# Optimization experiments

Hardware: AMD Instinct MI355X
Metric: run time of the kernel (lower is better)

## Reference

```python
import jax, jax.numpy as jnp
import numpy as np

SPARSE_DEGREE = 4   # MUL_LEV_SPA_ATN_SPARSE_DEGREES[level=1]
NUM_HEADS = 16


def setup_inputs() -> dict:
    key = jax.random.key(0)
    k1, k2, k3 = jax.random.split(key, 3)
    S, B, H, Dh = 4096, 2, NUM_HEADS, 128  # [seq, batch, heads, head_dim]
    q = jax.random.normal(k1, (S, B, H, Dh), jnp.float32)
    k = jax.random.normal(k2, (S, B, H, Dh), jnp.float32)
    v = jax.random.normal(k3, (S, B, H, Dh), jnp.float32)
    return {"q": q, "k": k, "v": v}


def reference(q, k, v):
    # Single-device (world_size=1) MLSAForOneLevel forward, is_prompt=True.
    d = SPARSE_DEGREE
    S, B, H, Dh = q.shape
    Ssp = S // d  # number of sparse tokens per head

    # Per-head strided indices: head h selects tokens h%d, h%d+d, ...  -> [Ssp, H]
    idx = (jnp.arange(H) % d)[None, :] + d * jnp.arange(Ssp)[:, None]
    idx4 = jnp.broadcast_to(idx[:, None, :, None], (Ssp, B, H, Dh))
    gather0 = lambda x: jnp.take_along_axis(x, idx4, axis=0)
    q_ = gather0(q)  # prompt phase: q is also sparsified
    k_ = gather0(k)
    v_ = gather0(v)

    # Core attention (causal), layout [t, b, h, d]
    scale = 1.0 / jnp.sqrt(jnp.asarray(Dh, q.dtype))
    scores = jnp.einsum('tbhd,sbhd->bhts', q_, k_) * scale  # [B,H,Ssp,Ssp]
    causal = jnp.tril(jnp.ones((Ssp, Ssp), bool))
    scores = jnp.where(causal[None, None], scores, -jnp.inf)
    m = jnp.max(scores, axis=-1, keepdims=True)
    e = jnp.exp(scores - m)
    denom = jnp.sum(e, axis=-1, keepdims=True)          # softmax denominator [B,H,Ssp,1]
    probs = e / denom
    ctx = jnp.einsum('bhts,sbhd->tbhd', probs, v_)       # [Ssp,B,H,Dh]

    # Reconstruction scatter: rc_indices[token, h] = i where token = i*d + h%d, else Ssp (-> zero row)
    rc = jnp.full((S, H), Ssp, jnp.int32)
    rc = rc.at[idx, jnp.arange(H)[None, :]].set(jnp.arange(Ssp, dtype=jnp.int32)[:, None])
    padded = jnp.concatenate([ctx, jnp.zeros((1, B, H, Dh), ctx.dtype)], axis=0)
    rc4 = jnp.broadcast_to(rc[:, None, :, None], (S, B, H, Dh))
    out = jnp.take_along_axis(padded, rc4, axis=0)       # [S,B,H,Dh]

    denomi = jnp.transpose(denom, (2, 0, 1, 3)).astype(jnp.float32)  # 'b h t x -> t b h x'
    return out, denomi
```

## Files before the change

kernel.cpp:

```cpp
#include <hip/hip_runtime.h>
#include <hip/hip_bf16.h>

typedef __attribute__((ext_vector_type(8))) __bf16 bf16x8;
typedef __attribute__((ext_vector_type(4))) float f32x4;

#define S_TOK 4096
#define NB 2
#define NH 16
#define DH 128
#define DEG 4
#define SSP 1024
#define QB 64
#define KB 64
#define NQT (SSP / QB)
#define TOKS (NB * NH * DH)
#define SCALE 0.08838834764831845f
#define VP 132

union U8 {
  bf16x8 v;
  unsigned u[4];
  unsigned short s[8];
};

__device__ __forceinline__ unsigned short f2bfu(float x) {
  __bf16 b = (__bf16)x;
  return __builtin_bit_cast(unsigned short, b);
}
__device__ __forceinline__ unsigned pkbf(float lo, float hi) {
  return (unsigned)f2bfu(lo) | ((unsigned)f2bfu(hi) << 16);
}

__global__ __launch_bounds__(256, 2) void mlsa_fused(
    const float* __restrict__ Qg, const float* __restrict__ Kg,
    const float* __restrict__ Vg, float* __restrict__ Og,
    float* __restrict__ Dg) {
  __shared__ __align__(16) char lds[KB * 256 + DH * VP];
  char* KL = lds;
  char* VT = lds + KB * 256;

  const int bid = blockIdx.x;
  const int jperm = bid >> 5;
  const int qt = (jperm < 8) ? jperm : 23 - jperm;
  const int bh = bid & 31;
  const int b = bh >> 4;
  const int h = bh & 15;
  const int hm4 = h & 3;
  const int tid = (int)threadIdx.x;
  const int wv = tid >> 6;
  const int ln = tid & 63;
  const int g = ln >> 4;
  const int c = ln & 15;
  const size_t bhoff = (size_t)b * (NH * DH) + (size_t)h * DH;

  const int qbase = qt * QB + wv * 16;
  const int q_sp = qbase + c;

  const int krow = tid >> 2;
  const int kd0 = (tid & 3) * 8;
  const int vd4 = tid & 31;
  const int vsp = tid >> 5;

  f32x4 qraw[8];
  {
    const float* qrow = Qg + (size_t)(q_sp * DEG + hm4) * TOKS + bhoff + g * 8;
    #pragma unroll
    for (int dc = 0; dc < 4; ++dc) {
      qraw[2 * dc] = *(const f32x4*)(qrow + dc * 32);
      qraw[2 * dc + 1] = *(const f32x4*)(qrow + dc * 32 + 4);
    }
  }
  f32x4 kreg[8], vreg[8];
  {
    const float* kr = Kg + (size_t)(krow * DEG + hm4) * TOKS + bhoff + kd0;
    #pragma unroll
    for (int p4 = 0; p4 < 4; ++p4) {
      kreg[2 * p4] = *(const f32x4*)(kr + p4 * 32);
      kreg[2 * p4 + 1] = *(const f32x4*)(kr + p4 * 32 + 4);
    }
    #pragma unroll
    for (int pp = 0; pp < 4; ++pp) {
      int s = pp * 16 + vsp * 2;
      const float* vr = Vg + (size_t)(s * DEG + hm4) * TOKS + bhoff + vd4 * 4;
      vreg[2 * pp] = *(const f32x4*)vr;
      vreg[2 * pp + 1] = *(const f32x4*)(vr + (size_t)DEG * TOKS);
    }
  }

  {
    const f32x4 z = {0.f, 0.f, 0.f, 0.f};
    for (int u = 0; u < 24; ++u) {
      int fid = u * 256 + tid;
      int row = fid >> 5;
      int col = fid & 31;
      int rr = row >> 6;
      int qi = qt * QB + (row & 63);
      int off = (hm4 + 1 + rr) & 3;
      *(f32x4*)(Og + (size_t)(qi * DEG + off) * TOKS + bhoff + col * 4) = z;
    }
  }

  bf16x8 qf[4];
  #pragma unroll
  for (int dc = 0; dc < 4; ++dc) {
    U8 t;
    #pragma unroll
    for (int i = 0; i < 4; ++i) {
      t.s[i] = f2bfu(qraw[2 * dc][i] * SCALE);
      t.s[4 + i] = f2bfu(qraw[2 * dc + 1][i] * SCALE);
    }
    qf[dc] = t.v;
  }

  U8 kpk[4];
  unsigned vpk[4][4];
  auto conv = [&]() {
    #pragma unroll
    for (int p4 = 0; p4 < 4; ++p4) {
      #pragma unroll
      for (int i = 0; i < 4; ++i) {
        kpk[p4].s[i] = f2bfu(kreg[2 * p4][i]);
        kpk[p4].s[4 + i] = f2bfu(kreg[2 * p4 + 1][i]);
      }
    }
    #pragma unroll
    for (int pp = 0; pp < 4; ++pp) {
      #pragma unroll
      for (int j = 0; j < 4; ++j)
        vpk[pp][j] = pkbf(vreg[2 * pp][j], vreg[2 * pp + 1][j]);
    }
  };
  auto wr = [&]() {
    #pragma unroll
    for (int p4 = 0; p4 < 4; ++p4) {
      int d = kd0 + p4 * 32;
      int byte = (krow * 256 + d * 2) ^ ((krow & 7) << 4);
      *(bf16x8*)(KL + byte) = kpk[p4].v;
    }
    #pragma unroll
    for (int pp = 0; pp < 4; ++pp) {
      int s = pp * 16 + vsp * 2;
      #pragma unroll
      for (int j = 0; j < 4; ++j)
        *(unsigned*)(VT + (vd4 * 4 + j) * VP + s * 2) = vpk[pp][j];
    }
  };

  conv();
  wr();
  __syncthreads();

  float m_run = -1e30f, m_true = -1e30f, l_run = 0.f;
  f32x4 acc[8];
  #pragma unroll
  for (int i = 0; i < 8; ++i) acc[i] = (f32x4){0.f, 0.f, 0.f, 0.f};

  for (int kt = 0; kt <= qt; ++kt) {
    const bool pf = (kt < qt);
    if (pf) {
      const float* kr =
          Kg + (size_t)(((kt + 1) * KB + krow) * DEG + hm4) * TOKS + bhoff + kd0;
      #pragma unroll
      for (int p4 = 0; p4 < 4; ++p4) {
        kreg[2 * p4] = *(const f32x4*)(kr + p4 * 32);
        kreg[2 * p4 + 1] = *(const f32x4*)(kr + p4 * 32 + 4);
      }
      #pragma unroll
      for (int pp = 0; pp < 4; ++pp) {
        int s = (kt + 1) * KB + pp * 16 + vsp * 2;
        const float* vr = Vg + (size_t)(s * DEG + hm4) * TOKS + bhoff + vd4 * 4;
        vreg[2 * pp] = *(const f32x4*)vr;
        vreg[2 * pp + 1] = *(const f32x4*)(vr + (size_t)DEG * TOKS);
      }
      __builtin_amdgcn_sched_barrier(0);
    }

    const int cbmax = pf ? 3 : wv;
    f32x4 sc[4];
    #pragma unroll
    for (int cb = 0; cb < 4; ++cb) sc[cb] = (f32x4){0.f, 0.f, 0.f, 0.f};
    #pragma unroll
    for (int cb = 0; cb < 4; ++cb) {
      if (cb <= cbmax) {
        int rbase = (cb * 16 + c) * 256;
        int sw = (c & 7) << 4;
        #pragma unroll
        for (int dc = 0; dc < 4; ++dc) {
          int byte = (rbase + (dc * 32 + g * 8) * 2) ^ sw;
          bf16x8 kf = *(const bf16x8*)(KL + byte);
          sc[cb] = __builtin_amdgcn_mfma_f32_16x16x32_bf16(kf, qf[dc], sc[cb], 0, 0, 0);
        }
      }
    }

    float p[4][4];
    float mt = -1e30f;
    if (pf) {
      #pragma unroll
      for (int cb = 0; cb < 4; ++cb) {
        #pragma unroll
        for (int r = 0; r < 4; ++r) {
          float v = sc[cb][r];
          p[cb][r] = v;
          mt = fmaxf(mt, v);
        }
      }
    } else {
      const int qloc = wv * 16 + c;
      #pragma unroll
      for (int cb = 0; cb < 4; ++cb) {
        #pragma unroll
        for (int r = 0; r < 4; ++r) {
          int kloc = cb * 16 + g * 4 + r;
          float v = (cb <= cbmax && kloc <= qloc) ? sc[cb][r] : -1e30f;
          p[cb][r] = v;
          mt = fmaxf(mt, v);
        }
      }
    }
    mt = fmaxf(mt, __shfl_xor(mt, 16));
    mt = fmaxf(mt, __shfl_xor(mt, 32));
    m_true = fmaxf(m_true, mt);

    float resc = 1.0f;
    if (!__all(mt <= m_run + 8.0f)) {
      float m_new = fmaxf(m_run, mt);
      resc = __expf(m_run - m_new);
      m_run = m_new;
      #pragma unroll
      for (int r = 0; r < 4; ++r) {
        float f = __shfl(resc, g * 4 + r);
        #pragma unroll
        for (int db = 0; db < 8; ++db) acc[db][r] *= f;
      }
    }
    float ls = 0.f;
    #pragma unroll
    for (int cb = 0; cb < 4; ++cb) {
      #pragma unroll
      for (int r = 0; r < 4; ++r) {
        float e = __expf(p[cb][r] - m_run);
        p[cb][r] = e;
        ls += e;
      }
    }
    ls += __shfl_xor(ls, 16);
    ls += __shfl_xor(ls, 32);
    l_run = l_run * resc + ls;

    unsigned pk2[4][2];
    #pragma unroll
    for (int cb = 0; cb < 4; ++cb) {
      pk2[cb][0] = pkbf(p[cb][0], p[cb][1]);
      pk2[cb][1] = pkbf(p[cb][2], p[cb][3]);
    }
    const int srcA = c + 16 * ((2 * g) & 3);
    const int srcB = c + 16 * ((2 * g + 1) & 3);
    const bool hi = (g & 2) != 0;
    const int sbmax = pf ? 1 : (wv >> 1);
    #pragma unroll
    for (int sb = 0; sb < 2; ++sb) {
      if (sb <= sbmax) {
        unsigned a0 = (unsigned)__shfl((int)pk2[2 * sb][0], srcA);
        unsigned b0 = (unsigned)__shfl((int)pk2[2 * sb + 1][0], srcA);
        unsigned a1 = (unsigned)__shfl((int)pk2[2 * sb][1], srcA);
        unsigned b1 = (unsigned)__shfl((int)pk2[2 * sb + 1][1], srcA);
        unsigned a2 = (unsigned)__shfl((int)pk2[2 * sb][0], srcB);
        unsigned b2 = (unsigned)__shfl((int)pk2[2 * sb + 1][0], srcB);
        unsigned a3 = (unsigned)__shfl((int)pk2[2 * sb][1], srcB);
        unsigned b3 = (unsigned)__shfl((int)pk2[2 * sb + 1][1], srcB);
        U8 pa;
        pa.u[0] = hi ? b0 : a0;
        pa.u[1] = hi ? b1 : a1;
        pa.u[2] = hi ? b2 : a2;
        pa.u[3] = hi ? b3 : a3;
        #pragma unroll
        for (int db = 0; db < 8; ++db) {
          int byte = (db * 16 + c) * VP + (sb * 32 + g * 8) * 2;
          U8 vb;
          vb.u[0] = *(const unsigned*)(VT + byte);
          vb.u[1] = *(const unsigned*)(VT + byte + 4);
          vb.u[2] = *(const unsigned*)(VT + byte + 8);
          vb.u[3] = *(const unsigned*)(VT + byte + 12);
          acc[db] = __builtin_amdgcn_mfma_f32_16x16x32_bf16(pa.v, vb.v, acc[db], 0, 0, 0);
        }
      }
    }

    if (!pf) break;
    conv();
    __syncthreads();
    wr();
    __syncthreads();
  }

  float inv = 1.0f / l_run;
  #pragma unroll
  for (int r = 0; r < 4; ++r) {
    float fi = __shfl(inv, g * 4 + r);
    int q2 = qbase + g * 4 + r;
    float* orow = Og + (size_t)(q2 * DEG + hm4) * TOKS + bhoff;
    #pragma unroll
    for (int db = 0; db < 8; ++db) orow[db * 16 + c] = acc[db][r] * fi;
  }
  if (g == 0)
    Dg[(size_t)(qbase + c) * (NB * NH) + b * NH + h] =
        l_run * __expf(m_run - m_true);
}

extern "C" void kernel_launch(void* const* d_in, const int* in_sizes, int n_in,
                              void* d_out, int out_size, void* d_ws, size_t ws_size,
                              hipStream_t stream) {
  (void)in_sizes; (void)n_in; (void)out_size; (void)d_ws; (void)ws_size;
  const float* q = (const float*)d_in[0];
  const float* k = (const float*)d_in[1];
  const float* v = (const float*)d_in[2];
  float* out = (float*)d_out;
  float* den = out + (size_t)S_TOK * NB * NH * DH;
  mlsa_fused<<<dim3(NQT * NB * NH), dim3(256), 0, stream>>>(q, k, v, out, den);
}
```

Measured before the change: 208.4 us.

## Split head dim across blocks, pair causal q-tiles, double-buffer K/V in LDS

Each block now handles one 64-wide half of the value head dimension and processes two causal query tiles (j and 15-j) back to back, which balances work per block. K/V staging moves to a double-buffered LDS layout, so each iteration needs one barrier instead of two, and the first K/V tile for the second phase is prefetched. The trade-off is that QK^T scores are computed twice, once per dh-half. That doubles QK MFMA work and K loads in exchange for better balance and overlap.

```diff
diff --git a/kernel.cpp b/kernel.cpp
--- a/kernel.cpp
+++ b/kernel.cpp
@@ -12,10 +12,12 @@
 #define SSP 1024
 #define QB 64
 #define KB 64
-#define NQT (SSP / QB)
 #define TOKS (NB * NH * DH)
 #define SCALE 0.08838834764831845f
-#define VP 132
+#define VP 148
+#define KSZ (KB * 256)
+#define VSZ (64 * VP)
+#define BUFSZ (KSZ + VSZ)
 
 union U8 {
   bf16x8 v;
@@ -35,14 +37,12 @@
     const float* __restrict__ Qg, const float* __restrict__ Kg,
     const float* __restrict__ Vg, float* __restrict__ Og,
     float* __restrict__ Dg) {
-  __shared__ __align__(16) char lds[KB * 256 + DH * VP];
-  char* KL = lds;
-  char* VT = lds + KB * 256;
+  __shared__ __align__(16) char lds[2 * BUFSZ];
 
   const int bid = blockIdx.x;
-  const int jperm = bid >> 5;
-  const int qt = (jperm < 8) ? jperm : 23 - jperm;
   const int bh = bid & 31;
+  const int j = (bid >> 5) & 7;
+  const int dhv = bid >> 8;
   const int b = bh >> 4;
   const int h = bh & 15;
   const int hm4 = h & 3;
@@ -52,68 +52,34 @@
   const int g = ln >> 4;
   const int c = ln & 15;
   const size_t bhoff = (size_t)b * (NH * DH) + (size_t)h * DH;
-
-  const int qbase = qt * QB + wv * 16;
-  const int q_sp = qbase + c;
+  const int dbase = dhv * 64;
 
   const int krow = tid >> 2;
   const int kd0 = (tid & 3) * 8;
-  const int vd4 = tid & 31;
-  const int vsp = tid >> 5;
-
-  f32x4 qraw[8];
-  {
-    const float* qrow = Qg + (size_t)(q_sp * DEG + hm4) * TOKS + bhoff + g * 8;
-    #pragma unroll
-    for (int dc = 0; dc < 4; ++dc) {
-      qraw[2 * dc] = *(const f32x4*)(qrow + dc * 32);
-      qraw[2 * dc + 1] = *(const f32x4*)(qrow + dc * 32 + 4);
-    }
-  }
-  f32x4 kreg[8], vreg[8];
-  {
-    const float* kr = Kg + (size_t)(krow * DEG + hm4) * TOKS + bhoff + kd0;
+  const int vd4 = tid & 15;
+  const int vsp = tid >> 4;
+
+  f32x4 kreg[8], vreg[4];
+  auto issue_kv = [&](int kt) {
+    const float* kr =
+        Kg + (size_t)((kt * KB + krow) * DEG + hm4) * TOKS + bhoff + kd0;
     #pragma unroll
     for (int p4 = 0; p4 < 4; ++p4) {
       kreg[2 * p4] = *(const f32x4*)(kr + p4 * 32);
       kreg[2 * p4 + 1] = *(const f32x4*)(kr + p4 * 32 + 4);
     }
     #pragma unroll
-    for (int pp = 0; pp < 4; ++pp) {
-      int s = pp * 16 + vsp * 2;
-      const float* vr = Vg + (size_t)(s * DEG + hm4) * TOKS + bhoff + vd4 * 4;
+    for (int pp = 0; pp < 2; ++pp) {
+      int s = kt * KB + pp * 32 + vsp * 2;
+      const float* vr =
+          Vg + (size_t)(s * DEG + hm4) * TOKS + bhoff + dbase + vd4 * 4;
       vreg[2 * pp] = *(const f32x4*)vr;
       vreg[2 * pp + 1] = *(const f32x4*)(vr + (size_t)DEG * TOKS);
     }
-  }
-
-  {
-    const f32x4 z = {0.f, 0.f, 0.f, 0.f};
-    for (int u = 0; u < 24; ++u) {
-      int fid = u * 256 + tid;
-      int row = fid >> 5;
-      int col = fid & 31;
-      int rr = row >> 6;
-      int qi = qt * QB + (row & 63);
-      int off = (hm4 + 1 + rr) & 3;
-      *(f32x4*)(Og + (size_t)(qi * DEG + off) * TOKS + bhoff + col * 4) = z;
-    }
-  }
-
-  bf16x8 qf[4];
-  #pragma unroll
-  for (int dc = 0; dc < 4; ++dc) {
-    U8 t;
-    #pragma unroll
-    for (int i = 0; i < 4; ++i) {
-      t.s[i] = f2bfu(qraw[2 * dc][i] * SCALE);
-      t.s[4 + i] = f2bfu(qraw[2 * dc + 1][i] * SCALE);
-    }
-    qf[dc] = t.v;
-  }
+  };
 
   U8 kpk[4];
-  unsigned vpk[4][4];
+  unsigned vpk[2][4];
   auto conv = [&]() {
     #pragma unroll
     for (int p4 = 0; p4 < 4; ++p4) {
@@ -124,13 +90,15 @@
       }
     }
     #pragma unroll
-    for (int pp = 0; pp < 4; ++pp) {
-      #pragma unroll
-      for (int j = 0; j < 4; ++j)
-        vpk[pp][j] = pkbf(vreg[2 * pp][j], vreg[2 * pp + 1][j]);
+    for (int pp = 0; pp < 2; ++pp) {
+      #pragma unroll
+      for (int jj = 0; jj < 4; ++jj)
+        vpk[pp][jj] = pkbf(vreg[2 * pp][jj], vreg[2 * pp + 1][jj]);
     }
   };
-  auto wr = [&]() {
+  auto wr = [&](int buf) {
+    char* KL = lds + buf * BUFSZ;
+    char* VT = KL + KSZ;
     #pragma unroll
     for (int p4 = 0; p4 < 4; ++p4) {
       int d = kd0 + p4 * 32;
@@ -138,174 +106,221 @@
       *(bf16x8*)(KL + byte) = kpk[p4].v;
     }
     #pragma unroll
-    for (int pp = 0; pp < 4; ++pp) {
-      int s = pp * 16 + vsp * 2;
-      #pragma unroll
-      for (int j = 0; j < 4; ++j)
-        *(unsigned*)(VT + (vd4 * 4 + j) * VP + s * 2) = vpk[pp][j];
+    for (int pp = 0; pp < 2; ++pp) {
+      int s2 = (pp * 32 + vsp * 2) * 2;
+      #pragma unroll
+      for (int jj = 0; jj < 4; ++jj)
+        *(unsigned*)(VT + (vd4 * 4 + jj) * VP + s2) = vpk[pp][jj];
     }
   };
 
-  conv();
-  wr();
-  __syncthreads();
-
-  float m_run = -1e30f, m_true = -1e30f, l_run = 0.f;
-  f32x4 acc[8];
-  #pragma unroll
-  for (int i = 0; i < 8; ++i) acc[i] = (f32x4){0.f, 0.f, 0.f, 0.f};
-
-  for (int kt = 0; kt <= qt; ++kt) {
-    const bool pf = (kt < qt);
-    if (pf) {
-      const float* kr =
-          Kg + (size_t)(((kt + 1) * KB + krow) * DEG + hm4) * TOKS + bhoff + kd0;
-      #pragma unroll
-      for (int p4 = 0; p4 < 4; ++p4) {
-        kreg[2 * p4] = *(const f32x4*)(kr + p4 * 32);
-        kreg[2 * p4 + 1] = *(const f32x4*)(kr + p4 * 32 + 4);
-      }
-      #pragma unroll
-      for (int pp = 0; pp < 4; ++pp) {
-        int s = (kt + 1) * KB + pp * 16 + vsp * 2;
-        const float* vr = Vg + (size_t)(s * DEG + hm4) * TOKS + bhoff + vd4 * 4;
-        vreg[2 * pp] = *(const f32x4*)vr;
-        vreg[2 * pp + 1] = *(const f32x4*)(vr + (size_t)DEG * TOKS);
-      }
-      __builtin_amdgcn_sched_barrier(0);
-    }
-
-    const int cbmax = pf ? 3 : wv;
-    f32x4 sc[4];
-    #pragma unroll
-    for (int cb = 0; cb < 4; ++cb) sc[cb] = (f32x4){0.f, 0.f, 0.f, 0.f};
-    #pragma unroll
-    for (int cb = 0; cb < 4; ++cb) {
-      if (cb <= cbmax) {
-        int rbase = (cb * 16 + c) * 256;
-        int sw = (c & 7) << 4;
+  int cur = 0;
+
+  for (int ph = 0; ph < 2; ++ph) {
+    const int qt = ph ? (15 - j) : j;
+    const int qbase = qt * QB + wv * 16;
+    const int q_sp = qbase + c;
+
+    f32x4 qraw[8];
+    {
+      const float* qrow =
+          Qg + (size_t)(q_sp * DEG + hm4) * TOKS + bhoff + g * 8;
+      #pragma unroll
+      for (int dc = 0; dc < 4; ++dc) {
+        qraw[2 * dc] = *(const f32x4*)(qrow + dc * 32);
+        qraw[2 * dc + 1] = *(const f32x4*)(qrow + dc * 32 + 4);
+      }
+    }
+
+    if (ph == 0) {
+      issue_kv(0);
+      const f32x4 z = {0.f, 0.f, 0.f, 0.f};
+      for (int u = 0; u < 24; ++u) {
+        int fid = u * 256 + tid;
+        int col = fid & 15;
+        int row = fid >> 4;
+        int t2 = row >= 192;
+        int r2 = row - (t2 ? 192 : 0);
+        int rr = r2 >> 6;
+        int qi = (t2 ? (15 - j) : j) * QB + (r2 & 63);
+        int off = (hm4 + 1 + rr) & 3;
+        *(f32x4*)(Og + (size_t)(qi * DEG + off) * TOKS + bhoff + dbase +
+                  col * 4) = z;
+      }
+    }
+
+    bf16x8 qf[4];
+    #pragma unroll
+    for (int dc = 0; dc < 4; ++dc) {
+      U8 t;
+      #pragma unroll
+      for (int i = 0; i < 4; ++i) {
+        t.s[i] = f2bfu(qraw[2 * dc][i] * SCALE);
+        t.s[4 + i] = f2bfu(qraw[2 * dc + 1][i] * SCALE);
+      }
+      qf[dc] = t.v;
+    }
+
+    if (ph == 0) {
+      conv();
+      wr(0);
+      __syncthreads();
+      cur = 0;
+    }
+
+    float m_run = -1e30f, m_true = -1e30f, l_run = 0.f;
+    f32x4 acc[4];
+    #pragma unroll
+    for (int i = 0; i < 4; ++i) acc[i] = (f32x4){0.f, 0.f, 0.f, 0.f};
+
+    for (int kt = 0; kt <= qt; ++kt) {
+      const bool diag = (kt == qt);
+      const bool has_next = (kt < qt) || (ph == 0);
+      if (has_next) {
+        issue_kv(diag ? 0 : kt + 1);
+        __builtin_amdgcn_sched_barrier(0);
+      }
+
+      const char* KL = lds + cur * BUFSZ;
+      const char* VT = KL + KSZ;
+
+      const int cbmax = diag ? wv : 3;
+      f32x4 sc[4];
+      #pragma unroll
+      for (int cb = 0; cb < 4; ++cb) sc[cb] = (f32x4){0.f, 0.f, 0.f, 0.f};
+      #pragma unroll
+      for (int cb = 0; cb < 4; ++cb) {
+        if (cb <= cbmax) {
+          int rbase = (cb * 16 + c) * 256;
+          int sw = (c & 7) << 4;
+          #pragma unroll
+          for (int dc = 0; dc < 4; ++dc) {
+            int byte = (rbase + (dc * 32 + g * 8) * 2) ^ sw;
+            bf16x8 kf = *(const bf16x8*)(KL + byte);
+            sc[cb] =
+                __builtin_amdgcn_mfma_f32_16x16x32_bf16(kf, qf[dc], sc[cb], 0, 0, 0);
+          }
+        }
+      }
+
+      float p[4][4];
+      float mt = -1e30f;
+      if (!diag) {
         #pragma unroll
-        for (int dc = 0; dc < 4; ++dc) {
-          int byte = (rbase + (dc * 32 + g * 8) * 2) ^ sw;
-          bf16x8 kf = *(const bf16x8*)(KL + byte);
-          sc[cb] = __builtin_amdgcn_mfma_f32_16x16x32_bf16(kf, qf[dc], sc[cb], 0, 0, 0);
-        }
-      }
-    }
-
-    float p[4][4];
-    float mt = -1e30f;
-    if (pf) {
+        for (int cb = 0; cb < 4; ++cb) {
+          #pragma unroll
+          for (int r = 0; r < 4; ++r) {
+            float v = sc[cb][r];
+            p[cb][r] = v;
+            mt = fmaxf(mt, v);
+          }
+        }
+      } else {
+        const int qloc = wv * 16 + c;
+        #pragma unroll
+        for (int cb = 0; cb < 4; ++cb) {
+          #pragma unroll
+          for (int r = 0; r < 4; ++r) {
+            int kloc = cb * 16 + g * 4 + r;
+            float v = (cb <= cbmax && kloc <= qloc) ? sc[cb][r] : -1e30f;
+            p[cb][r] = v;
+            mt = fmaxf(mt, v);
+          }
+        }
+      }
+      mt = fmaxf(mt, __shfl_xor(mt, 16));
+      mt = fmaxf(mt, __shfl_xor(mt, 32));
+      m_true = fmaxf(m_true, mt);
+
+      float resc = 1.0f;
+      if (!__all(mt <= m_run + 8.0f)) {
+        float m_new = fmaxf(m_run, mt);
+        resc = __expf(m_run - m_new);
+        m_run = m_new;
+        #pragma unroll
+        for (int r = 0; r < 4; ++r) {
+          float f = __shfl(resc, g * 4 + r);
+          #pragma unroll
+          for (int db = 0; db < 4; ++db) acc[db][r] *= f;
+        }
+      }
+      float ls = 0.f;
       #pragma unroll
       for (int cb = 0; cb < 4; ++cb) {
         #pragma unroll
         for (int r = 0; r < 4; ++r) {
-          float v = sc[cb][r];
-          p[cb][r] = v;
-          mt = fmaxf(mt, v);
-        }
-      }
-    } else {
-      const int qloc = wv * 16 + c;
+          float e = __expf(p[cb][r] - m_run);
+          p[cb][r] = e;
+          ls += e;
+        }
+      }
+      ls += __shfl_xor(ls, 16);
+      ls += __shfl_xor(ls, 32);
+      l_run = l_run * resc + ls;
+
+      unsigned pk2[4][2];
       #pragma unroll
       for (int cb = 0; cb < 4; ++cb) {
-        #pragma unroll
-        for (int r = 0; r < 4; ++r) {
-          int kloc = cb * 16 + g * 4 + r;
-          float v = (cb <= cbmax && kloc <= qloc) ? sc[cb][r] : -1e30f;
-          p[cb][r] = v;
-          mt = fmaxf(mt, v);
-        }
-      }
-    }
-    mt = fmaxf(mt, __shfl_xor(mt, 16));
-    mt = fmaxf(mt, __shfl_xor(mt, 32));
-    m_true = fmaxf(m_true, mt);
-
-    float resc = 1.0f;
-    if (!__all(mt <= m_run + 8.0f)) {
-      float m_new = fmaxf(m_run, mt);
-      resc = __expf(m_run - m_new);
-      m_run = m_new;
-      #pragma unroll
-      for (int r = 0; r < 4; ++r) {
-        float f = __shfl(resc, g * 4 + r);
-        #pragma unroll
-        for (int db = 0; db < 8; ++db) acc[db][r] *= f;
-      }
-    }
-    float ls = 0.f;
-    #pragma unroll
-    for (int cb = 0; cb < 4; ++cb) {
-      #pragma unroll
-      for (int r = 0; r < 4; ++r) {
-        float e = __expf(p[cb][r] - m_run);
-        p[cb][r] = e;
-        ls += e;
-      }
-    }
-    ls += __shfl_xor(ls, 16);
-    ls += __shfl_xor(ls, 32);
-    l_run = l_run * resc + ls;
-
-    unsigned pk2[4][2];
-    #pragma unroll
-    for (int cb = 0; cb < 4; ++cb) {
-      pk2[cb][0] = pkbf(p[cb][0], p[cb][1]);
-      pk2[cb][1] = pkbf(p[cb][2], p[cb][3]);
-    }
-    const int srcA = c + 16 * ((2 * g) & 3);
-    const int srcB = c + 16 * ((2 * g + 1) & 3);
-    const bool hi = (g & 2) != 0;
-    const int sbmax = pf ? 1 : (wv >> 1);
-    #pragma unroll
-    for (int sb = 0; sb < 2; ++sb) {
-      if (sb <= sbmax) {
-        unsigned a0 = (unsigned)__shfl((int)pk2[2 * sb][0], srcA);
-        unsigned b0 = (unsigned)__shfl((int)pk2[2 * sb + 1][0], srcA);
-        unsigned a1 = (unsigned)__shfl((int)pk2[2 * sb][1], srcA);
-        unsigned b1 = (unsigned)__shfl((int)pk2[2 * sb + 1][1], srcA);
-        unsigned a2 = (unsigned)__shfl((int)pk2[2 * sb][0], srcB);
-        unsigned b2 = (unsigned)__shfl((int)pk2[2 * sb + 1][0], srcB);
-        unsigned a3 = (unsigned)__shfl((int)pk2[2 * sb][1], srcB);
-        unsigned b3 = (unsigned)__shfl((int)pk2[2 * sb + 1][1], srcB);
-        U8 pa;
-        pa.u[0] = hi ? b0 : a0;
-        pa.u[1] = hi ? b1 : a1;
-        pa.u[2] = hi ? b2 : a2;
-        pa.u[3] = hi ? b3 : a3;
-        #pragma unroll
-        for (int db = 0; db < 8; ++db) {
-          int byte = (db * 16 + c) * VP + (sb * 32 + g * 8) * 2;
-          U8 vb;
-          vb.u[0] = *(const unsigned*)(VT + byte);
-          vb.u[1] = *(const unsigned*)(VT + byte + 4);
-          vb.u[2] = *(const unsigned*)(VT + byte + 8);
-          vb.u[3] = *(const unsigned*)(VT + byte + 12);
-          acc[db] = __builtin_amdgcn_mfma_f32_16x16x32_bf16(pa.v, vb.v, acc[db], 0, 0, 0);
-        }
-      }
-    }
-
-    if (!pf) break;
-    conv();
-    __syncthreads();
-    wr();
-    __syncthreads();
+        pk2[cb][0] = pkbf(p[cb][0], p[cb][1]);
+        pk2[cb][1] = pkbf(p[cb][2], p[cb][3]);
+      }
+      const int srcA = c + 16 * ((2 * g) & 3);
+      const int srcB = c + 16 * ((2 * g + 1) & 3);
+      const bool hi = (g & 2) != 0;
+
+      if (has_next) conv();
+
+      const int sbmax = diag ? (wv >> 1) : 1;
+      #pragma unroll
+      for (int sb = 0; sb < 2; ++sb) {
+        if (sb <= sbmax) {
+          unsigned a0 = (unsigned)__shfl((int)pk2[2 * sb][0], srcA);
+          unsigned b0 = (unsigned)__shfl((int)pk2[2 * sb + 1][0], srcA);
+          unsigned a1 = (unsigned)__shfl((int)pk2[2 * sb][1], srcA);
+          unsigned b1 = (unsigned)__shfl((int)pk2[2 * sb + 1][1], srcA);
+          unsigned a2 = (unsigned)__shfl((int)pk2[2 * sb][0], srcB);
+          unsigned b2 = (unsigned)__shfl((int)pk2[2 * sb + 1][0], srcB);
+          unsigned a3 = (unsigned)__shfl((int)pk2[2 * sb][1], srcB);
+          unsigned b3 = (unsigned)__shfl((int)pk2[2 * sb + 1][1], srcB);
+          U8 pa;
+          pa.u[0] = hi ? b0 : a0;
+          pa.u[1] = hi ? b1 : a1;
+          pa.u[2] = hi ? b2 : a2;
+          pa.u[3] = hi ? b3 : a3;
+          #pragma unroll
+          for (int db = 0; db < 4; ++db) {
+            int byte = (db * 16 + c) * VP + (sb * 32 + g * 8) * 2;
+            U8 vb;
+            vb.u[0] = *(const unsigned*)(VT + byte);
+            vb.u[1] = *(const unsigned*)(VT + byte + 4);
+            vb.u[2] = *(const unsigned*)(VT + byte + 8);
+            vb.u[3] = *(const unsigned*)(VT + byte + 12);
+            acc[db] =
+                __builtin_amdgcn_mfma_f32_16x16x32_bf16(pa.v, vb.v, acc[db], 0, 0, 0);
+          }
+        }
+      }
+
+      if (has_next) {
+        wr(cur ^ 1);
+        __syncthreads();
+      }
+      cur ^= 1;
+    }
+
+    float inv = 1.0f / l_run;
+    #pragma unroll
+    for (int r = 0; r < 4; ++r) {
+      float fi = __shfl(inv, g * 4 + r);
+      int q2 = qbase + g * 4 + r;
+      float* orow = Og + (size_t)(q2 * DEG + hm4) * TOKS + bhoff + dbase;
+      #pragma unroll
+      for (int db = 0; db < 4; ++db) orow[db * 16 + c] = acc[db][r] * fi;
+    }
+    if (g == 0 && dhv == 0)
+      Dg[(size_t)(qbase + c) * (NB * NH) + b * NH + h] =
+          l_run * __expf(m_run - m_true);
   }
-
-  float inv = 1.0f / l_run;
-  #pragma unroll
-  for (int r = 0; r < 4; ++r) {
-    float fi = __shfl(inv, g * 4 + r);
-    int q2 = qbase + g * 4 + r;
-    float* orow = Og + (size_t)(q2 * DEG + hm4) * TOKS + bhoff;
-    #pragma unroll
-    for (int db = 0; db < 8; ++db) orow[db * 16 + c] = acc[db][r] * fi;
-  }
-  if (g == 0)
-    Dg[(size_t)(qbase + c) * (NB * NH) + b * NH + h] =
-        l_run * __expf(m_run - m_true);
 }
 
 extern "C" void kernel_launch(void* const* d_in, const int* in_sizes, int n_in,
@@ -317,5 +332,5 @@
   const float* v = (const float*)d_in[2];
   float* out = (float*)d_out;
   float* den = out + (size_t)S_TOK * NB * NH * DH;
-  mlsa_fused<<<dim3(NQT * NB * NH), dim3(256), 0, stream>>>(q, k, v, out, den);
+  mlsa_fused<<<dim3(512), dim3(256), 0, stream>>>(q, k, v, out, den);
 }
```

Measured after the change: 209.9 us. No clear change (+0.7%).
